# Kernel tuning notes

Hardware: AMD Instinct MI355X
Metric: run time of the kernel (lower is better)

## Reference

```python
import jax, jax.numpy as jnp
import numpy as np

K, D, B = 512, 64, 4096  # n_primitives, view_dim, batch
TRIL_I, TRIL_J = np.tril_indices(D, -1)  # matches torch.tril_indices(D, D, offset=-1)
EPS = 1e-8


def setup_inputs() -> dict:
    key = jax.random.key(0)
    k1, k2, k3 = jax.random.split(key, 3)
    z = jax.random.normal(k1, (B, D), dtype=jnp.float32)
    # _init_weights: mu ~ N(0, 1/sqrt(D)) (random_normal mode)
    mu = jax.random.normal(k2, (K, D), dtype=jnp.float32) / np.float32(np.sqrt(D))
    # log_diag = 2*log(precision_init_scale) = 0 for scale=1, no jitter
    log_diag = jnp.zeros((K, D), dtype=jnp.float32)
    # point_softmax mode -> log_s zero-init
    log_s = jnp.zeros((K,), dtype=jnp.float32)
    # full covariance: lower_offdiag ~ N(0, offdiag_init_std=0.01)
    lower_offdiag = 0.01 * jax.random.normal(k3, (K, D * (D - 1) // 2), dtype=jnp.float32)
    return {"z": z, "mu": mu, "log_diag": log_diag, "log_s": log_s,
            "lower_offdiag": lower_offdiag}


def _precision_cholesky(log_diag, lower_offdiag):
    # (K, D, D) lower-triangular Cholesky factor of the precision matrix
    chol = jnp.zeros((K, D, D), dtype=log_diag.dtype)
    didx = jnp.arange(D)
    chol = chol.at[:, didx, didx].set(jnp.exp(0.5 * log_diag))
    chol = chol.at[:, TRIL_I, TRIL_J].set(lower_offdiag)
    return chol


def reference(z, mu, log_diag, log_s, lower_offdiag):
    chol = _precision_cholesky(log_diag, lower_offdiag)          # (K, D, D)
    diff = z[:, None, :] - mu[None, :, :]                        # (B, K, D)
    transformed = jnp.einsum('bkd,kde->bke', diff, chol)         # (B, K, D)
    mahal = jnp.sum(transformed * transformed, axis=-1)          # (B, K)
    strength = jax.nn.softplus(log_s)                            # (K,)
    log_a = -0.5 * mahal + jnp.log(strength + EPS)[None, :]
    log_a_max = jax.lax.stop_gradient(jnp.max(log_a, axis=-1, keepdims=True))
    a = jnp.exp(log_a - log_a_max)
    alpha = a / (jnp.sum(a, axis=-1, keepdims=True) + EPS)       # (B, K)
    return alpha
```

## Files before the change

### kernel.cpp

```cpp
#include <hip/hip_runtime.h>
#include <hip/hip_bf16.h>
#include <math.h>

#define KP   512
#define DD   64
#define BB   4096
#define NTRI 2016

typedef __attribute__((ext_vector_type(8))) short bfrag;
typedef __attribute__((ext_vector_type(4))) float facc4;


__device__ __forceinline__ void async16(const void* g, void* l) {
    __builtin_amdgcn_global_load_lds(
        (const __attribute__((address_space(1))) unsigned int*)g,
        (__attribute__((address_space(3))) unsigned int*)l, 16, 0, 0);
}

__global__ __launch_bounds__(256) void prep_kernel(
    const float* __restrict__ mu, const float* __restrict__ log_diag,
    const float* __restrict__ log_s, const float* __restrict__ lod,
    unsigned short* __restrict__ Limg, float* __restrict__ wws,
    float* __restrict__ biasws)
{
    const int k = blockIdx.x;
    const int tid = threadIdx.x;
    __shared__ float Lc[64 * 64];
    __shared__ float muS[64];

    for (int idx = tid; idx < 4096; idx += 256) Lc[idx] = 0.0f;
    if (tid < 64) muS[tid] = mu[k * 64 + tid];
    __syncthreads();

    if (tid < 64) Lc[tid * 64 + tid] = expf(0.5f * log_diag[k * 64 + tid]);
    for (int t = tid; t < NTRI; t += 256) {
        int i = (int)((1.0f + sqrtf(8.0f * (float)t + 1.0f)) * 0.5f);
        while (i * (i - 1) / 2 > t) --i;
        while ((i + 1) * i / 2 <= t) ++i;
        int j = t - i * (i - 1) / 2;
        Lc[j * 64 + i] = lod[(size_t)k * NTRI + t];
    }
    __syncthreads();

    if (tid < 64) {
        const int e = tid;
        float s = 0.0f;
        for (int d = e; d < 64; ++d) s += muS[d] * Lc[e * 64 + d];
        wws[k * 64 + e] = -s;
    }
    for (int idx = tid; idx < 4096; idx += 256) {
        int e = idx >> 6, d = idx & 63;
        int sw = (e << 6) | (d ^ ((e & 7) << 3));
        __hip_bfloat16 hb = __float2bfloat16(Lc[idx]);
        Limg[(size_t)k * 4096 + sw] = *(unsigned short*)&hb;
    }
    if (tid == 0) {
        float s = log_s[k];
        float sp = (s > 20.0f) ? s : log1pf(expf(s));
        biasws[k] = logf(sp + 1e-8f);
    }
}

__global__ __launch_bounds__(256) void mahal_kernel(
    const float* __restrict__ z, const unsigned short* __restrict__ Limg,
    const float* __restrict__ wws, float* __restrict__ mahal)
{
    __shared__ __align__(16) char  ldsImg[3][8192];
    __shared__ __align__(16) float wS[16 * 64];

    const int tid  = threadIdx.x;
    const int wave = tid >> 6;
    const int lane = tid & 63;
    const int g    = lane >> 4;
    const int l15  = lane & 15;

    const int n      = blockIdx.x;
    const int kslice = (n & 7) + ((n >> 7) << 3);
    const int bblk   = (n >> 3) & 15;
    const int k0     = kslice * 16;
    const int bw     = bblk * 256 + wave * 64;

    const char* imgK = (const char*)Limg + (size_t)k0 * 8192;

#pragma unroll
    for (int b0 = 0; b0 < 2; ++b0) {
        const char* src = imgK + (size_t)b0 * 8192;
        char* dst = &ldsImg[b0][0];
#pragma unroll
        for (int p = 0; p < 2; ++p) {
            const int cof = p * 4096 + wave * 1024;
            async16(src + cof + lane * 16, dst + cof);
        }
    }

    for (int i = tid; i < 16 * 64; i += 256) wS[i] = wws[k0 * 64 + i];

    bfrag zh[4][2], zl[4][2];
#pragma unroll
    for (int bs = 0; bs < 4; ++bs) {
        const float* zp = z + (size_t)(bw + bs * 16 + l15) * 64 + 8 * g;
#pragma unroll
        for (int ds = 0; ds < 2; ++ds) {
            float4 a = *(const float4*)(zp + ds * 32);
            float4 c = *(const float4*)(zp + ds * 32 + 4);
            float vv[8] = {a.x, a.y, a.z, a.w, c.x, c.y, c.z, c.w};
            bfrag th, tl;
#pragma unroll
            for (int j = 0; j < 8; ++j) {
                __hip_bfloat16 hb = __float2bfloat16(vv[j]);
                float hv = __bfloat162float(hb);
                __hip_bfloat16 lb = __float2bfloat16(vv[j] - hv);
                th[j] = *(short*)&hb;
                tl[j] = *(short*)&lb;
            }
            zh[bs][ds] = th;
            zl[bs][ds] = tl;
        }
    }

    const int swz = (l15 & 7) << 4;

    __syncthreads();

    for (int t = 0; t < 16; ++t) {
        __builtin_amdgcn_s_barrier();

        if (t + 2 < 16) {
            const char* src = imgK + (size_t)(t + 2) * 8192;
            char* dst = &ldsImg[(t + 2) % 3][0];
#pragma unroll
            for (int p = 0; p < 2; ++p) {
                const int cof = p * 4096 + wave * 1024;
                async16(src + cof + lane * 16, dst + cof);
            }
        }

        if (t < 14)       asm volatile("s_waitcnt vmcnt(12)" ::: "memory");
        else if (t == 14) asm volatile("s_waitcnt vmcnt(10)" ::: "memory");
        else              asm volatile("s_waitcnt vmcnt(8)"  ::: "memory");
        __builtin_amdgcn_s_barrier();

        const char* buf = &ldsImg[t % 3][0];

        const float* wrow = wS + t * 64;
        float4 wv[4];
#pragma unroll
        for (int et = 0; et < 4; ++et)
            wv[et] = *(const float4*)(wrow + et * 16 + 4 * g);

        facc4 acc[4][4];
#pragma unroll
        for (int et = 0; et < 4; ++et)
#pragma unroll
            for (int bs = 0; bs < 4; ++bs) {
                acc[et][bs][0] = wv[et].x;
                acc[et][bs][1] = wv[et].y;
                acc[et][bs][2] = wv[et].z;
                acc[et][bs][3] = wv[et].w;
            }

        __builtin_amdgcn_s_setprio(1);
#pragma unroll
        for (int ds = 0; ds < 2; ++ds) {
#pragma unroll
            for (int et = 0; et < 4; ++et) {
                if (et >= 2 && ds == 0) continue;
                const int ao = et * 2048 + l15 * 128 + ((ds * 64 + 16 * g) ^ swz);
                bfrag lh = *(const bfrag*)(buf + ao);
#pragma unroll
                for (int bs = 0; bs < 4; ++bs) {
                    acc[et][bs] = __builtin_amdgcn_mfma_f32_16x16x32_bf16(lh, zh[bs][ds], acc[et][bs], 0, 0, 0);
                    acc[et][bs] = __builtin_amdgcn_mfma_f32_16x16x32_bf16(lh, zl[bs][ds], acc[et][bs], 0, 0, 0);
                }
            }
        }
        __builtin_amdgcn_s_setprio(0);

        const int k = k0 + t;
#pragma unroll
        for (int bs = 0; bs < 4; ++bs) {
            float p0 = 0.f, p1 = 0.f, p2 = 0.f, p3 = 0.f;
#pragma unroll
            for (int et = 0; et < 4; ++et) {
                p0 = fmaf(acc[et][bs][0], acc[et][bs][0], p0);
                p1 = fmaf(acc[et][bs][1], acc[et][bs][1], p1);
                p2 = fmaf(acc[et][bs][2], acc[et][bs][2], p2);
                p3 = fmaf(acc[et][bs][3], acc[et][bs][3], p3);
            }
            float s = (p0 + p1) + (p2 + p3);
            s += __shfl_xor(s, 16, 64);
            s += __shfl_xor(s, 32, 64);
            if (g == 0)
                mahal[(size_t)(bw + bs * 16 + l15) * KP + k] = s;
        }
    }
}

__global__ __launch_bounds__(256) void softmax_kernel(
    const float* __restrict__ mahal, const float* __restrict__ biasws,
    float* __restrict__ alpha)
{
    const int tid  = threadIdx.x;
    const int lane = tid & 63;
    const int b    = blockIdx.x * 4 + (tid >> 6);

    const float* mrow = mahal + (size_t)b * KP + lane * 8;
    const float* brow = biasws + lane * 8;
    float4 m0 = *(const float4*)(mrow);
    float4 m1 = *(const float4*)(mrow + 4);
    float4 c0 = *(const float4*)(brow);
    float4 c1 = *(const float4*)(brow + 4);

    float la[8];
    la[0] = fmaf(-0.5f, m0.x, c0.x); la[1] = fmaf(-0.5f, m0.y, c0.y);
    la[2] = fmaf(-0.5f, m0.z, c0.z); la[3] = fmaf(-0.5f, m0.w, c0.w);
    la[4] = fmaf(-0.5f, m1.x, c1.x); la[5] = fmaf(-0.5f, m1.y, c1.y);
    la[6] = fmaf(-0.5f, m1.z, c1.z); la[7] = fmaf(-0.5f, m1.w, c1.w);

    float lm = la[0];
#pragma unroll
    for (int j = 1; j < 8; ++j) lm = fmaxf(lm, la[j]);
#pragma unroll
    for (int off = 32; off >= 1; off >>= 1)
        lm = fmaxf(lm, __shfl_xor(lm, off, 64));

    float a[8], s = 0.0f;
#pragma unroll
    for (int j = 0; j < 8; ++j) { a[j] = expf(la[j] - lm); s += a[j]; }
#pragma unroll
    for (int off = 32; off >= 1; off >>= 1)
        s += __shfl_xor(s, off, 64);

    const float r = 1.0f / (s + 1e-8f);
    float4 o0 = {a[0] * r, a[1] * r, a[2] * r, a[3] * r};
    float4 o1 = {a[4] * r, a[5] * r, a[6] * r, a[7] * r};
    float* orow = alpha + (size_t)b * KP + lane * 8;
    *(float4*)(orow)     = o0;
    *(float4*)(orow + 4) = o1;
}

extern "C" void kernel_launch(void* const* d_in, const int* in_sizes, int n_in,
                              void* d_out, int out_size, void* d_ws, size_t ws_size,
                              hipStream_t stream) {
    const float* z        = (const float*)d_in[0];
    const float* mu       = (const float*)d_in[1];
    const float* log_diag = (const float*)d_in[2];
    const float* log_s    = (const float*)d_in[3];
    const float* lod      = (const float*)d_in[4];
    float* out = (float*)d_out;

    char* ws = (char*)d_ws;
    unsigned short* Limg = (unsigned short*)ws;
    float* wws    = (float*)(ws + (size_t)KP * 8192);
    float* biasws = wws + (size_t)KP * 64;
    float* mahalws = biasws + KP;

    prep_kernel<<<KP, 256, 0, stream>>>(mu, log_diag, log_s, lod, Limg, wws, biasws);
    mahal_kernel<<<512, 256, 0, stream>>>(z, Limg, wws, mahalws);
    softmax_kernel<<<BB / 4, 256, 0, stream>>>(mahalws, biasws, out);
}
```

Baseline: 50.52 us.

## Give each wave a private double-buffered L tile to drop block barriers

The mahal kernel stops sharing a triple-buffered L image across the block. Each wave now streams its own full copy of every 8 KB L tile into a private double buffer, synchronised only with vmcnt waits. This removes the two block-wide barriers per iteration. In exchange, each wave loads four times as much L data from global/L2, and LDS per block grows to about 68 KB, which may cut occupancy. Separately, the prep kernel spreads the mu·L bias reduction over all 256 threads with a shared-memory partial-sum step.

```diff
diff --git a/kernel.cpp b/kernel.cpp
--- a/kernel.cpp
+++ b/kernel.cpp
@@ -27,6 +27,7 @@
     const int tid = threadIdx.x;
     __shared__ float Lc[64 * 64];
     __shared__ float muS[64];
+    __shared__ float wp[4][64];
 
     for (int idx = tid; idx < 4096; idx += 256) Lc[idx] = 0.0f;
     if (tid < 64) muS[tid] = mu[k * 64 + tid];
@@ -42,12 +43,17 @@
     }
     __syncthreads();
 
-    if (tid < 64) {
-        const int e = tid;
+    {
+        const int e = tid & 63, part = tid >> 6;
         float s = 0.0f;
-        for (int d = e; d < 64; ++d) s += muS[d] * Lc[e * 64 + d];
-        wws[k * 64 + e] = -s;
-    }
+        for (int d = e + part; d < 64; d += 4)
+            s += muS[d] * Lc[e * 64 + d];
+        wp[part][e] = s;
+    }
+    __syncthreads();
+    if (tid < 64)
+        wws[k * 64 + tid] = -(wp[0][tid] + wp[1][tid] + wp[2][tid] + wp[3][tid]);
+
     for (int idx = tid; idx < 4096; idx += 256) {
         int e = idx >> 6, d = idx & 63;
         int sw = (e << 6) | (d ^ ((e & 7) << 3));
@@ -65,7 +71,7 @@
     const float* __restrict__ z, const unsigned short* __restrict__ Limg,
     const float* __restrict__ wws, float* __restrict__ mahal)
 {
-    __shared__ __align__(16) char  ldsImg[3][8192];
+    __shared__ __align__(16) char  ldsImg[4][2][8192];
     __shared__ __align__(16) float wS[16 * 64];
 
     const int tid  = threadIdx.x;
@@ -81,17 +87,11 @@
     const int bw     = bblk * 256 + wave * 64;
 
     const char* imgK = (const char*)Limg + (size_t)k0 * 8192;
-
-#pragma unroll
-    for (int b0 = 0; b0 < 2; ++b0) {
-        const char* src = imgK + (size_t)b0 * 8192;
-        char* dst = &ldsImg[b0][0];
-#pragma unroll
-        for (int p = 0; p < 2; ++p) {
-            const int cof = p * 4096 + wave * 1024;
-            async16(src + cof + lane * 16, dst + cof);
-        }
-    }
+    char* myLds = &ldsImg[wave][0][0];
+
+#pragma unroll
+    for (int p = 0; p < 8; ++p)
+        async16(imgK + p * 1024 + lane * 16, myLds + p * 1024);
 
     for (int i = tid; i < 16 * 64; i += 256) wS[i] = wws[k0 * 64 + i];
 
@@ -123,24 +123,19 @@
     __syncthreads();
 
     for (int t = 0; t < 16; ++t) {
-        __builtin_amdgcn_s_barrier();
-
-        if (t + 2 < 16) {
-            const char* src = imgK + (size_t)(t + 2) * 8192;
-            char* dst = &ldsImg[(t + 2) % 3][0];
-#pragma unroll
-            for (int p = 0; p < 2; ++p) {
-                const int cof = p * 4096 + wave * 1024;
-                async16(src + cof + lane * 16, dst + cof);
-            }
-        }
-
-        if (t < 14)       asm volatile("s_waitcnt vmcnt(12)" ::: "memory");
-        else if (t == 14) asm volatile("s_waitcnt vmcnt(10)" ::: "memory");
-        else              asm volatile("s_waitcnt vmcnt(8)"  ::: "memory");
-        __builtin_amdgcn_s_barrier();
-
-        const char* buf = &ldsImg[t % 3][0];
+        if (t + 1 < 16) {
+            const char* src = imgK + (size_t)(t + 1) * 8192;
+            char* dst = myLds + ((t + 1) & 1) * 8192;
+#pragma unroll
+            for (int p = 0; p < 8; ++p)
+                async16(src + p * 1024 + lane * 16, dst + p * 1024);
+        }
+
+        if (t == 0)       asm volatile("s_waitcnt vmcnt(8)"  ::: "memory");
+        else if (t < 15)  asm volatile("s_waitcnt vmcnt(12)" ::: "memory");
+        else              asm volatile("s_waitcnt vmcnt(4)"  ::: "memory");
+
+        const char* buf = myLds + (t & 1) * 8192;
 
         const float* wrow = wS + t * 64;
         float4 wv[4];
```

New measurement: 50.09 us. Within noise of the previous version (-0.9%).
